# Kernel optimization log

Hardware: AMD Instinct MI355X
Metric: run time of the kernel (lower is better)

The kernel has to match this reference:

```python
import jax, jax.numpy as jnp
import numpy as np

B, T, C = 2, 2048, 2048
N_HEAD = 16
N_KV_HEAD = 16
HEAD_DIM = C // N_HEAD  # 128
KV_LORA = C // 2        # 1024
KV_PE = KV_LORA // 4    # 256
KV_CONTENT = KV_LORA - KV_PE  # 768
EPS = 1.1920929e-07  # torch.finfo(float32).eps, F.rms_norm default


def _rms_norm(x):
    # unlearned RMSNorm over last dim
    return x * jax.lax.rsqrt(jnp.mean(x * x, axis=-1, keepdims=True) + EPS)


def _apply_rotary(x, cos, sin):
    # x: (B,T,H,D); cos,sin: (1,T,1,D/2)
    d = x.shape[-1] // 2
    x1, x2 = x[..., :d], x[..., d:]
    return jnp.concatenate([x1 * cos + x2 * sin, -x1 * sin + x2 * cos], axis=-1)


def setup_inputs() -> dict:
    key = jax.random.key(0)
    ks = jax.random.split(key, 9)
    x = jax.random.normal(ks[0], (B, T, C), dtype=jnp.float32)
    # realistic RoPE tables (values bounded like real cos/sin)
    half = HEAD_DIM // 2
    inv_freq = 1.0 / (10000.0 ** (np.arange(0, half, dtype=np.float32) / half))
    tpos = np.arange(T, dtype=np.float32)
    ang = np.einsum('t,d->td', tpos, inv_freq)
    cos = jnp.asarray(np.cos(ang))[None, :, None, :]
    sin = jnp.asarray(np.sin(ang))[None, :, None, :]
    s = 0.02
    wq_a = jax.random.normal(ks[1], (C, KV_LORA), dtype=jnp.float32) * s
    wq_b = jax.random.normal(ks[2], (KV_LORA, N_HEAD * HEAD_DIM), dtype=jnp.float32) * s
    wkv_a = jax.random.normal(ks[3], (C, KV_LORA), dtype=jnp.float32) * s
    wk_b = jax.random.normal(ks[4], (KV_CONTENT, N_KV_HEAD * HEAD_DIM), dtype=jnp.float32) * s
    wkpe_b = jax.random.normal(ks[5], (KV_PE, N_KV_HEAD * HEAD_DIM), dtype=jnp.float32) * s
    wv_b = jax.random.normal(ks[6], (KV_CONTENT, N_KV_HEAD * HEAD_DIM), dtype=jnp.float32) * s
    wo = jax.random.normal(ks[7], (C, C), dtype=jnp.float32) * s
    return dict(x=x, cos=cos, sin=sin, wq_a=wq_a, wq_b=wq_b, wkv_a=wkv_a,
                wk_b=wk_b, wkpe_b=wkpe_b, wv_b=wv_b, wo=wo)


def reference(x, cos, sin, wq_a, wq_b, wkv_a, wk_b, wkpe_b, wv_b, wo):
    Bx, Tx, Cx = x.shape
    # low-rank Q path
    q = (x @ wq_a) @ wq_b                      # (B,T,H*D)
    q = q.reshape(Bx, Tx, N_HEAD, HEAD_DIM)
    # low-rank KV path with pe/content split
    kv_latent = x @ wkv_a                       # (B,T,KV_LORA)
    kv_pe = kv_latent[..., :KV_PE]
    kv_content = kv_latent[..., KV_PE:]
    k_content = (kv_content @ wk_b).reshape(Bx, Tx, N_KV_HEAD, HEAD_DIM)
    k_pe = (kv_pe @ wkpe_b).reshape(Bx, Tx, N_KV_HEAD, HEAD_DIM)
    k = k_content + _apply_rotary(k_pe, cos, sin)
    v = (kv_content @ wv_b).reshape(Bx, Tx, N_KV_HEAD, HEAD_DIM)
    # QK RMSNorm (unlearned)
    q = _rms_norm(q)
    k = _rms_norm(k)
    # SDPA, causal (kv_cache=None path); n_head == n_kv_head
    qh = q.transpose(0, 2, 1, 3)  # (B,H,T,D)
    kh = k.transpose(0, 2, 1, 3)
    vh = v.transpose(0, 2, 1, 3)
    scale = 1.0 / jnp.sqrt(jnp.asarray(HEAD_DIM, dtype=x.dtype))
    scores = jnp.einsum('bhqd,bhkd->bhqk', qh, kh) * scale
    causal = jnp.tril(jnp.ones((Tx, Tx), dtype=bool))
    scores = jnp.where(causal[None, None], scores, jnp.asarray(-jnp.inf, dtype=scores.dtype))
    probs = jax.nn.softmax(scores, axis=-1)
    y = jnp.einsum('bhqk,bhkd->bhqd', probs, vh)
    y = y.transpose(0, 2, 1, 3).reshape(Bx, Tx, Cx)
    return y @ wo
```

## Files before the change

### kernel.cpp

```cpp
#include <hip/hip_runtime.h>
#include <cstddef>
#include <cstdint>

#define TT 2048
#define HH 16
#define EPSV 1.1920929e-07f
#define QSCALE 0.08838834764831845f
#define LOG2E 1.4426950408889634f
#define THRL 11.0f

typedef short bfv8 __attribute__((ext_vector_type(8)));
typedef float f32x4 __attribute__((ext_vector_type(4)));

__device__ __forceinline__ short f2bf(float f) {
    unsigned u = __builtin_bit_cast(unsigned, f);
    u += 0x7FFFu + ((u >> 16) & 1u);
    return (short)(u >> 16);
}
__device__ __forceinline__ float bf2f(short s) {
    unsigned u = ((unsigned)(unsigned short)s) << 16;
    return __builtin_bit_cast(float, u);
}
__device__ __forceinline__ bfv8 pack8(const float4 a, const float4 b) {
    bfv8 r;
    r[0]=f2bf(a.x); r[1]=f2bf(a.y); r[2]=f2bf(a.z); r[3]=f2bf(a.w);
    r[4]=f2bf(b.x); r[5]=f2bf(b.y); r[6]=f2bf(b.z); r[7]=f2bf(b.w);
    return r;
}
__device__ __forceinline__ void gload16(const void* g, void* l) {
    __builtin_amdgcn_global_load_lds(
        (const __attribute__((address_space(1))) unsigned int*)g,
        (__attribute__((address_space(3))) unsigned int*)l, 16, 0, 0);
}
__device__ __forceinline__ unsigned cvtpk(float a, float b) {
    unsigned r;
    asm("v_cvt_pk_bf16_f32 %0, %1, %2" : "=v"(r) : "v"(a), "v"(b));
    return r;
}
__device__ __forceinline__ float fexp2(float x) {
    float y;
    asm volatile("v_exp_f32 %0, %1\n\ts_nop 1" : "=v"(y) : "v"(x));
    return y;
}
#define SWZF(V, IMM) __builtin_bit_cast(float, __builtin_amdgcn_ds_swizzle(__builtin_bit_cast(int, (V)), IMM))
#define RMAX_RND(M, IMM) { M[0]=fmaxf(M[0],SWZF(M[0],IMM)); M[1]=fmaxf(M[1],SWZF(M[1],IMM)); \
                           M[2]=fmaxf(M[2],SWZF(M[2],IMM)); M[3]=fmaxf(M[3],SWZF(M[3],IMM)); }
#define RMAX4(M) RMAX_RND(M,0x041F) RMAX_RND(M,0x081F) RMAX_RND(M,0x101F) RMAX_RND(M,0x201F)
#define RSUM_RND(M, IMM) { M[0]+=SWZF(M[0],IMM); M[1]+=SWZF(M[1],IMM); \
                           M[2]+=SWZF(M[2],IMM); M[3]+=SWZF(M[3],IMM); }
#define RSUM4(M) RSUM_RND(M,0x041F) RSUM_RND(M,0x081F) RSUM_RND(M,0x101F) RSUM_RND(M,0x201F)

__global__ __launch_bounds__(256) void convx(const float* __restrict__ src,
                                             short* __restrict__ dst, int n8)
{
    int i = blockIdx.x * blockDim.x + threadIdx.x;
    int stride = gridDim.x * blockDim.x;
    for (; i < n8; i += stride) {
        float4 a = ((const float4*)src)[2*i], b = ((const float4*)src)[2*i+1];
        ((bfv8*)dst)[i] = pack8(a, b);
    }
}

__global__ __launch_bounds__(256) void wtrans(const float* __restrict__ src,
                                              short* __restrict__ dst, int R, int C)
{
    __shared__ short tile[64][72];
    const int tid = threadIdx.x;
    const int r0 = blockIdx.y * 64, c0 = blockIdx.x * 64;
    {
        const int i = tid >> 2, c = (tid & 3) * 16;
        const float* sp = src + ((size_t)(r0 + i)) * C + c0 + c;
        float4 v0 = ((const float4*)sp)[0], v1 = ((const float4*)sp)[1];
        float4 v2 = ((const float4*)sp)[2], v3 = ((const float4*)sp)[3];
        *(bfv8*)&tile[i][c]     = pack8(v0, v1);
        *(bfv8*)&tile[i][c + 8] = pack8(v2, v3);
    }
    __syncthreads();
    {
        const int j = tid >> 2, rc = (tid & 3) * 16;
        bfv8 g0, g1;
#pragma unroll
        for (int jj = 0; jj < 8; ++jj) { g0[jj] = tile[rc + jj][j]; g1[jj] = tile[rc + 8 + jj][j]; }
        short* dp = dst + ((size_t)(c0 + j)) * R + r0 + rc;
        *(bfv8*)dp       = g0;
        *(bfv8*)(dp + 8) = g1;
    }
}

template<int OUT_MODE>
__global__ __launch_bounds__(256) void gemm_bf16(
    const short* __restrict__ A, int lda,
    const short* __restrict__ B, int ldb,
    void* __restrict__ Cptr, int ldc, int K)
{
    __shared__ short As[2][128 * 32];
    __shared__ short Bs[2][128 * 32];
    const int tid = threadIdx.x;
    const int w = tid >> 6, lane = tid & 63;
    const int lr = lane & 15, lg = lane >> 4;
    const int wr = w >> 1, wc = w & 1;
    const size_t bm = (size_t)blockIdx.y * 128, bn = (size_t)blockIdx.x * 128;

    f32x4 acc[4][4] = {};

    const int r0 = tid >> 2, ch = (tid & 3) * 8;
    const short* aB0 = A + (bm + r0) * (size_t)lda + ch;
    const short* aB1 = aB0 + 64 * (size_t)lda;
    const short* bB0 = B + (bn + r0) * (size_t)ldb + ch;
    const short* bB1 = bB0 + 64 * (size_t)ldb;
    const int wof = w * 512;

    gload16(aB0, As[0] + wof);
    gload16(aB1, As[0] + wof + 2048);
    gload16(bB0, Bs[0] + wof);
    gload16(bB1, Bs[0] + wof + 2048);
    __syncthreads();

    int cur = 0;
    for (int k0 = 0; k0 < K; k0 += 32) {
        if (k0 + 32 < K) {
            gload16(aB0 + k0 + 32, As[cur ^ 1] + wof);
            gload16(aB1 + k0 + 32, As[cur ^ 1] + wof + 2048);
            gload16(bB0 + k0 + 32, Bs[cur ^ 1] + wof);
            gload16(bB1 + k0 + 32, Bs[cur ^ 1] + wof + 2048);
        }
        bfv8 af[4], bfr[4];
#pragma unroll
        for (int i = 0; i < 4; ++i) {
            af[i]  = *(const bfv8*)&As[cur][(wr * 64 + i * 16 + lr) * 32 + lg * 8];
            bfr[i] = *(const bfv8*)&Bs[cur][(wc * 64 + i * 16 + lr) * 32 + lg * 8];
        }
#pragma unroll
        for (int i = 0; i < 4; ++i)
#pragma unroll
            for (int j = 0; j < 4; ++j)
                acc[i][j] = __builtin_amdgcn_mfma_f32_16x16x32_bf16(af[i], bfr[j], acc[i][j], 0, 0, 0);
        __syncthreads();
        cur ^= 1;
    }

    const size_t crow = bm + wr * 64 + 4 * lg;
    const size_t ccol = bn + wc * 64 + lr;
#pragma unroll
    for (int i = 0; i < 4; ++i)
#pragma unroll
        for (int j = 0; j < 4; ++j)
#pragma unroll
            for (int r = 0; r < 4; ++r) {
                size_t off = (crow + i * 16 + r) * (size_t)ldc + ccol + j * 16;
                if (OUT_MODE == 0) ((float*)Cptr)[off] = acc[i][j][r];
                else               ((short*)Cptr)[off] = f2bf(acc[i][j][r]);
            }
}

__global__ __launch_bounds__(256) void finalize_k(
    const short* __restrict__ kc, const short* __restrict__ pe,
    const float* __restrict__ cosb, const float* __restrict__ sinb,
    short* __restrict__ kb)
{
    const int gw = blockIdx.x * 4 + (threadIdx.x >> 6);
    const int l = threadIdx.x & 63;
    const int r = gw >> 4, h = gw & 15;
    const int t = r & (TT - 1), b = r >> 11;
    const size_t kcb = (size_t)r * 4096 + h * 128;
    const size_t peb = (size_t)r * 2048 + h * 128;

    float x1 = bf2f(pe[peb + l]), x2 = bf2f(pe[peb + 64 + l]);
    float c = cosb[t * 64 + l], s = sinb[t * 64 + l];
    float lo = bf2f(kc[kcb + l])      + x1 * c + x2 * s;
    float hi = bf2f(kc[kcb + 64 + l]) - x1 * s + x2 * c;

    float ss = lo * lo + hi * hi;
#pragma unroll
    for (int o = 32; o; o >>= 1) ss += __shfl_xor(ss, o);
    float rr = rsqrtf(ss * (1.0f / 128.0f) + EPSV);
    const size_t ob = (((size_t)b * HH + h) * TT + t) * 128;
    kb[ob + l]      = f2bf(lo * rr);
    kb[ob + 64 + l] = f2bf(hi * rr);
}

__global__ __launch_bounds__(256) void vtrans(
    const short* __restrict__ src, short* __restrict__ dst)
{
    __shared__ short tile[64][72];
    const int tt = blockIdx.x, dt = blockIdx.y, bh = blockIdx.z;
    const int tid = threadIdx.x;
    {
        const int i = tid >> 2, c = (tid & 3) * 16;
        const size_t sb = ((size_t)((bh >> 4) * TT + tt * 64 + i)) * 4096 + 2048 + (bh & 15) * 128 + dt * 64 + c;
        *(bfv8*)&tile[i][c]     = *(const bfv8*)&src[sb];
        *(bfv8*)&tile[i][c + 8] = *(const bfv8*)&src[sb + 8];
    }
    __syncthreads();
    {
        const int j = tid >> 2, rc = (tid & 3) * 16;
        bfv8 g0, g1;
#pragma unroll
        for (int jj = 0; jj < 8; ++jj) { g0[jj] = tile[rc + jj][j]; g1[jj] = tile[rc + 8 + jj][j]; }
        const size_t db = (((size_t)bh) * 128 + dt * 64 + j) * TT + tt * 64 + rc;
        *(bfv8*)&dst[db]     = g0;
        *(bfv8*)&dst[db + 8] = g1;
    }
}

__device__ __forceinline__ void qk_tile(const short* __restrict__ Ks,
    const bfv8 aq[4], f32x4 s[4], int lr, int lg)
{
    const int swz = lr & 7;
#pragma unroll
    for (int ct = 0; ct < 4; ++ct) {
        f32x4 a = {0.f, 0.f, 0.f, 0.f};
        const int row = ct * 16 + lr;
#pragma unroll
        for (int ks = 0; ks < 4; ++ks) {
            const bfv8 bk = *(const bfv8*)&Ks[row * 128 + (((ks * 4 + lg) ^ swz) * 8)];
            a = __builtin_amdgcn_mfma_f32_16x16x32_bf16(aq[ks], bk, a, 0, 0, 0);
        }
        s[ct] = a;
    }
}

__device__ __forceinline__ void mask_diag(f32x4 s[4], int lr, int lg, int w)
{
    const int rq = w * 16 + 4 * lg;
#pragma unroll
    for (int ct = 0; ct < 4; ++ct)
#pragma unroll
        for (int r = 0; r < 4; ++r)
            if (ct * 16 + lr > rq + r) s[ct][r] = -__builtin_inff();
}

__device__ __forceinline__ void softmax1(f32x4 s[4], float m[4], float l[4], f32x4 o[8])
{
    float mt[4];
#pragma unroll
    for (int r = 0; r < 4; ++r) mt[r] = fmaxf(fmaxf(s[0][r], s[1][r]), fmaxf(s[2][r], s[3][r]));
    RMAX4(mt)
    float g = fmaxf(fmaxf(mt[0] - m[0], mt[1] - m[1]), fmaxf(mt[2] - m[2], mt[3] - m[3]));
    if (!__all(g <= THRL)) {
        float alpha[4];
#pragma unroll
        for (int r = 0; r < 4; ++r) {
            float mn = fmaxf(m[r], mt[r]);
            alpha[r] = fexp2(m[r] - mn);
            m[r] = mn; l[r] *= alpha[r];
        }
#pragma unroll
        for (int dt = 0; dt < 8; ++dt) {
            o[dt][0] *= alpha[0]; o[dt][1] *= alpha[1];
            o[dt][2] *= alpha[2]; o[dt][3] *= alpha[3];
        }
    }
#pragma unroll
    for (int ct = 0; ct < 4; ++ct)
#pragma unroll
        for (int r = 0; r < 4; ++r) s[ct][r] = fexp2(s[ct][r] - m[r]);
    float rs[4];
#pragma unroll
    for (int r = 0; r < 4; ++r) rs[r] = (s[0][r] + s[1][r]) + (s[2][r] + s[3][r]);
    RSUM4(rs)
#pragma unroll
    for (int r = 0; r < 4; ++r) l[r] += rs[r];
}

__device__ __forceinline__ void softmax2(
    f32x4 s1[4], f32x4 s2[4],
    float m1[4], float l1[4], float m2[4], float l2[4],
    f32x4 o1[8], f32x4 o2[8])
{
    float mt1[4], mt2[4];
#pragma unroll
    for (int r = 0; r < 4; ++r) {
        mt1[r] = fmaxf(fmaxf(s1[0][r], s1[1][r]), fmaxf(s1[2][r], s1[3][r]));
        mt2[r] = fmaxf(fmaxf(s2[0][r], s2[1][r]), fmaxf(s2[2][r], s2[3][r]));
    }
    RMAX4(mt1) RMAX4(mt2)
    float g1 = fmaxf(fmaxf(mt1[0] - m1[0], mt1[1] - m1[1]), fmaxf(mt1[2] - m1[2], mt1[3] - m1[3]));
    float g2 = fmaxf(fmaxf(mt2[0] - m2[0], mt2[1] - m2[1]), fmaxf(mt2[2] - m2[2], mt2[3] - m2[3]));
    if (!__all(g1 <= THRL)) {
        float alpha[4];
#pragma unroll
        for (int r = 0; r < 4; ++r) {
            float mn = fmaxf(m1[r], mt1[r]);
            alpha[r] = fexp2(m1[r] - mn);
            m1[r] = mn; l1[r] *= alpha[r];
        }
#pragma unroll
        for (int dt = 0; dt < 8; ++dt) {
            o1[dt][0] *= alpha[0]; o1[dt][1] *= alpha[1];
            o1[dt][2] *= alpha[2]; o1[dt][3] *= alpha[3];
        }
    }
    if (!__all(g2 <= THRL)) {
        float alpha[4];
#pragma unroll
        for (int r = 0; r < 4; ++r) {
            float mn = fmaxf(m2[r], mt2[r]);
            alpha[r] = fexp2(m2[r] - mn);
            m2[r] = mn; l2[r] *= alpha[r];
        }
#pragma unroll
        for (int dt = 0; dt < 8; ++dt) {
            o2[dt][0] *= alpha[0]; o2[dt][1] *= alpha[1];
            o2[dt][2] *= alpha[2]; o2[dt][3] *= alpha[3];
        }
    }
#pragma unroll
    for (int ct = 0; ct < 4; ++ct)
#pragma unroll
        for (int r = 0; r < 4; ++r) {
            s1[ct][r] = fexp2(s1[ct][r] - m1[r]);
            s2[ct][r] = fexp2(s2[ct][r] - m2[r]);
        }
    float rs1[4], rs2[4];
#pragma unroll
    for (int r = 0; r < 4; ++r) {
        rs1[r] = (s1[0][r] + s1[1][r]) + (s1[2][r] + s1[3][r]);
        rs2[r] = (s2[0][r] + s2[1][r]) + (s2[2][r] + s2[3][r]);
    }
    RSUM4(rs1) RSUM4(rs2)
#pragma unroll
    for (int r = 0; r < 4; ++r) { l1[r] += rs1[r]; l2[r] += rs2[r]; }
}

__device__ __forceinline__ void pv_tile(const short* __restrict__ Vs,
    short (&Psw)[16][72], const f32x4 s[4], f32x4 o[8], int lr, int lg)
{
#pragma unroll
    for (int ct = 0; ct < 4; ++ct) {
        unsigned u0 = cvtpk(s[ct][0], s[ct][1]);
        unsigned u1 = cvtpk(s[ct][2], s[ct][3]);
        Psw[4 * lg + 0][ct * 16 + lr] = (short)u0;
        Psw[4 * lg + 1][ct * 16 + lr] = (short)(u0 >> 16);
        Psw[4 * lg + 2][ct * 16 + lr] = (short)u1;
        Psw[4 * lg + 3][ct * 16 + lr] = (short)(u1 >> 16);
    }
    const bfv8 pa0 = *(const bfv8*)&Psw[lr][lg * 8];
    const bfv8 pa1 = *(const bfv8*)&Psw[lr][32 + lg * 8];
    const int swz = lr & 7;
#pragma unroll
    for (int dt = 0; dt < 8; ++dt) {
        const int row = dt * 16 + lr;
        const bfv8 bv0 = *(const bfv8*)&Vs[row * 64 + ((lg ^ swz) * 8)];
        const bfv8 bv1 = *(const bfv8*)&Vs[row * 64 + (((4 + lg) ^ swz) * 8)];
        o[dt] = __builtin_amdgcn_mfma_f32_16x16x32_bf16(pa0, bv0, o[dt], 0, 0, 0);
        o[dt] = __builtin_amdgcn_mfma_f32_16x16x32_bf16(pa1, bv1, o[dt], 0, 0, 0);
    }
}

__global__ __launch_bounds__(256) void attn_kernel(
    const short* __restrict__ qg, const short* __restrict__ kg,
    const short* __restrict__ vg, short* __restrict__ y)
{
    __shared__ short Ks[64 * 128];
    __shared__ short Vs[128 * 64];
    __shared__ short Ps[4][16][72];

    const int lin = blockIdx.x + 16 * blockIdx.y + 256 * blockIdx.z;
    const int work = (lin & 7) * 64 + (lin >> 3);
    const int pi = work & 15, h = (work >> 4) & 15, b = work >> 8;
    const int qt1 = pi, qt2 = 31 - pi;
    const int tid = threadIdx.x, w = tid >> 6, lane = tid & 63;
    const int lr = lane & 15, lg = lane >> 4;

    const size_t tok0 = ((size_t)b * HH + h) * TT;

    bfv8 aq1[4], aq2[4];
    {
        const size_t q1 = ((size_t)b * TT + qt1 * 64 + w * 16 + lr) * 2048 + h * 128;
        const size_t q2 = ((size_t)b * TT + qt2 * 64 + w * 16 + lr) * 2048 + h * 128;
#pragma unroll
        for (int ks = 0; ks < 4; ++ks) {
            aq1[ks] = *(const bfv8*)&qg[q1 + ks * 32 + lg * 8];
            aq2[ks] = *(const bfv8*)&qg[q2 + ks * 32 + lg * 8];
        }
#pragma unroll
        for (int st = 0; st < 2; ++st) {
            bfv8* aq = st ? aq2 : aq1;
            float ss = 0.f;
#pragma unroll
            for (int ks = 0; ks < 4; ++ks)
#pragma unroll
                for (int j = 0; j < 8; ++j) { float f = bf2f(aq[ks][j]); ss = fmaf(f, f, ss); }
            ss += __shfl_xor(ss, 16);
            ss += __shfl_xor(ss, 32);
            float rr = rsqrtf(ss * (1.0f / 128.0f) + EPSV) * (QSCALE * LOG2E);
#pragma unroll
            for (int ks = 0; ks < 4; ++ks)
#pragma unroll
                for (int j = 0; j < 4; ++j) {
                    unsigned u = cvtpk(bf2f(aq[ks][2 * j]) * rr, bf2f(aq[ks][2 * j + 1]) * rr);
                    aq[ks][2 * j]     = (short)u;
                    aq[ks][2 * j + 1] = (short)(u >> 16);
                }
        }
    }

    f32x4 o1[8] = {}; f32x4 o2[8] = {};
    float m1[4], l1[4], m2[4], l2[4];
#pragma unroll
    for (int r = 0; r < 4; ++r) { m1[r] = m2[r] = -__builtin_inff(); l1[r] = l2[r] = 0.f; }

    const size_t vhead = ((size_t)b * HH + h) * (size_t)128 * TT;
    const int krow = tid >> 4, kub = (tid & 15) ^ (krow & 7);
    const int vrow = tid >> 3, vub = (tid & 7) ^ (vrow & 7);
    const int wof = w * 512;

    for (int kt = 0; kt <= qt2; ++kt) {
        {
            const size_t kbase = (tok0 + kt * 64) * 128;
#pragma unroll
            for (int p = 0; p < 4; ++p) {
                gload16(kg + kbase + (p * 16 + krow) * 128 + kub * 8, Ks + wof + p * 2048);
                gload16(vg + vhead + (size_t)(p * 32 + vrow) * TT + kt * 64 + vub * 8,
                        Vs + wof + p * 2048);
            }
        }
        __syncthreads();

        if (kt <= qt1) {
            f32x4 s1[4], s2[4];
            qk_tile(Ks, aq2, s2, lr, lg);
            qk_tile(Ks, aq1, s1, lr, lg);
            if (kt == qt1) mask_diag(s1, lr, lg, w);
            softmax2(s1, s2, m1, l1, m2, l2, o1, o2);
            pv_tile(Vs, Ps[w], s2, o2, lr, lg);
            pv_tile(Vs, Ps[w], s1, o1, lr, lg);
        } else {
            f32x4 s2[4];
            qk_tile(Ks, aq2, s2, lr, lg);
            if (kt == qt2) mask_diag(s2, lr, lg, w);
            softmax1(s2, m2, l2, o2);
            pv_tile(Vs, Ps[w], s2, o2, lr, lg);
        }
        __syncthreads();
    }

#pragma unroll
    for (int r = 0; r < 4; ++r) {
        float inv1 = 1.0f / l1[r], inv2 = 1.0f / l2[r];
        const size_t y1 = ((size_t)b * TT + qt1 * 64 + w * 16 + 4 * lg + r) * 2048 + h * 128 + lr;
        const size_t y2 = ((size_t)b * TT + qt2 * 64 + w * 16 + 4 * lg + r) * 2048 + h * 128 + lr;
#pragma unroll
        for (int dt = 0; dt < 8; ++dt) {
            y[y1 + dt * 16] = f2bf(o1[dt][r] * inv1);
            y[y2 + dt * 16] = f2bf(o2[dt][r] * inv2);
        }
    }
}

extern "C" void kernel_launch(void* const* d_in, const int* in_sizes, int n_in,
                              void* d_out, int out_size, void* d_ws, size_t ws_size,
                              hipStream_t stream)
{
    const float* x      = (const float*)d_in[0];
    const float* cosb   = (const float*)d_in[1];
    const float* sinb   = (const float*)d_in[2];
    const float* wq_a   = (const float*)d_in[3];
    const float* wq_b   = (const float*)d_in[4];
    const float* wkv_a  = (const float*)d_in[5];
    const float* wk_b   = (const float*)d_in[6];
    const float* wkpe_b = (const float*)d_in[7];
    const float* wv_b   = (const float*)d_in[8];
    const float* wo     = (const float*)d_in[9];

    short* wsp = (short*)d_ws;
    short* W1  = wsp;
    short* W2  = wsp + 4194304;
    short* W3  = wsp + 7340032;
    short* W4  = wsp + 7864320;
    short* W5  = wsp + 9961472;
    short* C1  = wsp + 14155776;
    short* KV2 = wsp + 22544384;
    short* KPE = wsp + 39321600;
    short* KB  = wsp + 47710208;
    short* VB  = wsp + 56098816;
    short* XB  = (short*)d_out;

    dim3 blk(256);

    convx<<<2048, blk, 0, stream>>>(x, XB, 1048576);
    wtrans<<<dim3(16, 32), blk, 0, stream>>>(wq_a,   W1,                2048, 1024);
    wtrans<<<dim3(16, 32), blk, 0, stream>>>(wkv_a,  W1 + 1024 * 2048,  2048, 1024);
    wtrans<<<dim3(32, 12), blk, 0, stream>>>(wk_b,   W2,                 768, 2048);
    wtrans<<<dim3(32, 12), blk, 0, stream>>>(wv_b,   W2 + 2048 * 768,    768, 2048);
    wtrans<<<dim3(32,  4), blk, 0, stream>>>(wkpe_b, W3,                 256, 2048);
    wtrans<<<dim3(32, 16), blk, 0, stream>>>(wq_b,   W4,                1024, 2048);
    wtrans<<<dim3(32, 32), blk, 0, stream>>>(wo,     W5,                2048, 2048);

    gemm_bf16<1><<<dim3(16, 32), blk, 0, stream>>>(XB, 2048, W1, 2048, C1, 2048, 2048);
    gemm_bf16<1><<<dim3(32, 32), blk, 0, stream>>>(C1 + 1280, 2048, W2, 768, KV2, 4096, 768);
    gemm_bf16<1><<<dim3(16, 32), blk, 0, stream>>>(C1 + 1024, 2048, W3, 256, KPE, 2048, 256);

    finalize_k<<<16384, blk, 0, stream>>>(KV2, KPE, cosb, sinb, KB);
    vtrans<<<dim3(32, 2, 32), blk, 0, stream>>>(KV2, VB);

    gemm_bf16<1><<<dim3(16, 32), blk, 0, stream>>>(C1, 2048, W4, 1024, KPE, 2048, 1024);

    attn_kernel<<<dim3(16, 16, 2), blk, 0, stream>>>(KPE, KB, VB, C1);

    gemm_bf16<0><<<dim3(16, 32), blk, 0, stream>>>(C1, 2048, W5, 2048, d_out, 2048, 2048);
}
```

Before: 348.9 us.

## Transpose QK MFMA so each lane owns one query row in softmax

The QK^T MFMA operands are swapped so the score tile comes out transposed, with each lane holding one query row across four key columns. Row max and sum then need only two cross-lane shuffles instead of four swizzle rounds per row, and P is stored to LDS as packed 4-element vectors. The rescale factors and final normalisers are redistributed to the O-accumulator layout with ds_bpermute. Separate P buffers per query tile let both PV products run interleaved in one loop, which adds LDS use and extra permutes on rescale.

```diff
diff --git a/kernel.cpp b/kernel.cpp
--- a/kernel.cpp
+++ b/kernel.cpp
@@ -10,7 +10,9 @@
 #define THRL 11.0f
 
 typedef short bfv8 __attribute__((ext_vector_type(8)));
+typedef short bfv4 __attribute__((ext_vector_type(4)));
 typedef float f32x4 __attribute__((ext_vector_type(4)));
+typedef unsigned u32x2 __attribute__((ext_vector_type(2)));
 
 __device__ __forceinline__ short f2bf(float f) {
     unsigned u = __builtin_bit_cast(unsigned, f);
@@ -42,13 +44,14 @@
     asm volatile("v_exp_f32 %0, %1\n\ts_nop 1" : "=v"(y) : "v"(x));
     return y;
 }
-#define SWZF(V, IMM) __builtin_bit_cast(float, __builtin_amdgcn_ds_swizzle(__builtin_bit_cast(int, (V)), IMM))
-#define RMAX_RND(M, IMM) { M[0]=fmaxf(M[0],SWZF(M[0],IMM)); M[1]=fmaxf(M[1],SWZF(M[1],IMM)); \
-                           M[2]=fmaxf(M[2],SWZF(M[2],IMM)); M[3]=fmaxf(M[3],SWZF(M[3],IMM)); }
-#define RMAX4(M) RMAX_RND(M,0x041F) RMAX_RND(M,0x081F) RMAX_RND(M,0x101F) RMAX_RND(M,0x201F)
-#define RSUM_RND(M, IMM) { M[0]+=SWZF(M[0],IMM); M[1]+=SWZF(M[1],IMM); \
-                           M[2]+=SWZF(M[2],IMM); M[3]+=SWZF(M[3],IMM); }
-#define RSUM4(M) RSUM_RND(M,0x041F) RSUM_RND(M,0x081F) RSUM_RND(M,0x101F) RSUM_RND(M,0x201F)
+__device__ __forceinline__ float bperm(float v, int addr) {
+    return __builtin_bit_cast(float,
+        __builtin_amdgcn_ds_bpermute(addr, __builtin_bit_cast(int, v)));
+}
+__device__ __forceinline__ bfv4 mkfrag(float a, float b, float c, float d) {
+    u32x2 t; t[0] = cvtpk(a, b); t[1] = cvtpk(c, d);
+    return __builtin_bit_cast(bfv4, t);
+}
 
 __global__ __launch_bounds__(256) void convx(const float* __restrict__ src,
                                              short* __restrict__ dst, int n8)
@@ -203,7 +206,25 @@
     }
 }
 
-__device__ __forceinline__ void qk_tile(const short* __restrict__ Ks,
+__device__ __forceinline__ void qk_dual(const short* __restrict__ Ks,
+    const bfv8 aq1[4], const bfv8 aq2[4], f32x4 s1[4], f32x4 s2[4], int lr, int lg)
+{
+    const int swz = lr & 7;
+#pragma unroll
+    for (int ct = 0; ct < 4; ++ct) {
+        f32x4 a1 = {0.f, 0.f, 0.f, 0.f}, a2 = {0.f, 0.f, 0.f, 0.f};
+        const int row = ct * 16 + lr;
+#pragma unroll
+        for (int ks = 0; ks < 4; ++ks) {
+            const bfv8 bk = *(const bfv8*)&Ks[row * 128 + (((ks * 4 + lg) ^ swz) * 8)];
+            a1 = __builtin_amdgcn_mfma_f32_16x16x32_bf16(bk, aq1[ks], a1, 0, 0, 0);
+            a2 = __builtin_amdgcn_mfma_f32_16x16x32_bf16(bk, aq2[ks], a2, 0, 0, 0);
+        }
+        s1[ct] = a1; s2[ct] = a2;
+    }
+}
+
+__device__ __forceinline__ void qk_one(const short* __restrict__ Ks,
     const bfv8 aq[4], f32x4 s[4], int lr, int lg)
 {
     const int swz = lr & 7;
@@ -214,7 +235,7 @@
 #pragma unroll
         for (int ks = 0; ks < 4; ++ks) {
             const bfv8 bk = *(const bfv8*)&Ks[row * 128 + (((ks * 4 + lg) ^ swz) * 8)];
-            a = __builtin_amdgcn_mfma_f32_16x16x32_bf16(aq[ks], bk, a, 0, 0, 0);
+            a = __builtin_amdgcn_mfma_f32_16x16x32_bf16(bk, aq[ks], a, 0, 0, 0);
         }
         s[ct] = a;
     }
@@ -222,121 +243,86 @@
 
 __device__ __forceinline__ void mask_diag(f32x4 s[4], int lr, int lg, int w)
 {
-    const int rq = w * 16 + 4 * lg;
+    const int qq = w * 16 + lr;
 #pragma unroll
     for (int ct = 0; ct < 4; ++ct)
 #pragma unroll
         for (int r = 0; r < 4; ++r)
-            if (ct * 16 + lr > rq + r) s[ct][r] = -__builtin_inff();
-}
-
-__device__ __forceinline__ void softmax1(f32x4 s[4], float m[4], float l[4], f32x4 o[8])
-{
-    float mt[4];
-#pragma unroll
-    for (int r = 0; r < 4; ++r) mt[r] = fmaxf(fmaxf(s[0][r], s[1][r]), fmaxf(s[2][r], s[3][r]));
-    RMAX4(mt)
-    float g = fmaxf(fmaxf(mt[0] - m[0], mt[1] - m[1]), fmaxf(mt[2] - m[2], mt[3] - m[3]));
-    if (!__all(g <= THRL)) {
-        float alpha[4];
-#pragma unroll
-        for (int r = 0; r < 4; ++r) {
-            float mn = fmaxf(m[r], mt[r]);
-            alpha[r] = fexp2(m[r] - mn);
-            m[r] = mn; l[r] *= alpha[r];
-        }
+            if (ct * 16 + 4 * lg + r > qq) s[ct][r] = -__builtin_inff();
+}
+
+__device__ __forceinline__ void softmax_lane(f32x4 s[4], float& m, float& l,
+                                             f32x4 o[8], int a0)
+{
+    float c0 = fmaxf(fmaxf(s[0][0], s[0][1]), fmaxf(s[0][2], s[0][3]));
+    float c1 = fmaxf(fmaxf(s[1][0], s[1][1]), fmaxf(s[1][2], s[1][3]));
+    float c2 = fmaxf(fmaxf(s[2][0], s[2][1]), fmaxf(s[2][2], s[2][3]));
+    float c3 = fmaxf(fmaxf(s[3][0], s[3][1]), fmaxf(s[3][2], s[3][3]));
+    float mt = fmaxf(fmaxf(c0, c1), fmaxf(c2, c3));
+    mt = fmaxf(mt, __shfl_xor(mt, 16));
+    mt = fmaxf(mt, __shfl_xor(mt, 32));
+    if (!__all(mt - m <= THRL)) {
+        float mn = fmaxf(m, mt);
+        float alpha = fexp2(m - mn);
+        m = mn;
+        l *= alpha;
+        float av0 = bperm(alpha, a0);
+        float av1 = bperm(alpha, a0 + 4);
+        float av2 = bperm(alpha, a0 + 8);
+        float av3 = bperm(alpha, a0 + 12);
 #pragma unroll
         for (int dt = 0; dt < 8; ++dt) {
-            o[dt][0] *= alpha[0]; o[dt][1] *= alpha[1];
-            o[dt][2] *= alpha[2]; o[dt][3] *= alpha[3];
-        }
-    }
+            o[dt][0] *= av0; o[dt][1] *= av1;
+            o[dt][2] *= av2; o[dt][3] *= av3;
+        }
+    }
+    f32x4 acc = {0.f, 0.f, 0.f, 0.f};
+#pragma unroll
+    for (int ct = 0; ct < 4; ++ct) {
+#pragma unroll
+        for (int r = 0; r < 4; ++r) s[ct][r] = fexp2(s[ct][r] - m);
+        acc += s[ct];
+    }
+    float rs = (acc[0] + acc[1]) + (acc[2] + acc[3]);
+    rs += __shfl_xor(rs, 16);
+    rs += __shfl_xor(rs, 32);
+    l += rs;
+}
+
+__device__ __forceinline__ void p_store(short (&Psw)[16][72], const f32x4 s[4],
+                                        int lr, int lg)
+{
 #pragma unroll
     for (int ct = 0; ct < 4; ++ct)
-#pragma unroll
-        for (int r = 0; r < 4; ++r) s[ct][r] = fexp2(s[ct][r] - m[r]);
-    float rs[4];
-#pragma unroll
-    for (int r = 0; r < 4; ++r) rs[r] = (s[0][r] + s[1][r]) + (s[2][r] + s[3][r]);
-    RSUM4(rs)
-#pragma unroll
-    for (int r = 0; r < 4; ++r) l[r] += rs[r];
-}
-
-__device__ __forceinline__ void softmax2(
-    f32x4 s1[4], f32x4 s2[4],
-    float m1[4], float l1[4], float m2[4], float l2[4],
-    f32x4 o1[8], f32x4 o2[8])
-{
-    float mt1[4], mt2[4];
-#pragma unroll
-    for (int r = 0; r < 4; ++r) {
-        mt1[r] = fmaxf(fmaxf(s1[0][r], s1[1][r]), fmaxf(s1[2][r], s1[3][r]));
-        mt2[r] = fmaxf(fmaxf(s2[0][r], s2[1][r]), fmaxf(s2[2][r], s2[3][r]));
-    }
-    RMAX4(mt1) RMAX4(mt2)
-    float g1 = fmaxf(fmaxf(mt1[0] - m1[0], mt1[1] - m1[1]), fmaxf(mt1[2] - m1[2], mt1[3] - m1[3]));
-    float g2 = fmaxf(fmaxf(mt2[0] - m2[0], mt2[1] - m2[1]), fmaxf(mt2[2] - m2[2], mt2[3] - m2[3]));
-    if (!__all(g1 <= THRL)) {
-        float alpha[4];
-#pragma unroll
-        for (int r = 0; r < 4; ++r) {
-            float mn = fmaxf(m1[r], mt1[r]);
-            alpha[r] = fexp2(m1[r] - mn);
-            m1[r] = mn; l1[r] *= alpha[r];
-        }
-#pragma unroll
-        for (int dt = 0; dt < 8; ++dt) {
-            o1[dt][0] *= alpha[0]; o1[dt][1] *= alpha[1];
-            o1[dt][2] *= alpha[2]; o1[dt][3] *= alpha[3];
-        }
-    }
-    if (!__all(g2 <= THRL)) {
-        float alpha[4];
-#pragma unroll
-        for (int r = 0; r < 4; ++r) {
-            float mn = fmaxf(m2[r], mt2[r]);
-            alpha[r] = fexp2(m2[r] - mn);
-            m2[r] = mn; l2[r] *= alpha[r];
-        }
-#pragma unroll
-        for (int dt = 0; dt < 8; ++dt) {
-            o2[dt][0] *= alpha[0]; o2[dt][1] *= alpha[1];
-            o2[dt][2] *= alpha[2]; o2[dt][3] *= alpha[3];
-        }
-    }
-#pragma unroll
-    for (int ct = 0; ct < 4; ++ct)
-#pragma unroll
-        for (int r = 0; r < 4; ++r) {
-            s1[ct][r] = fexp2(s1[ct][r] - m1[r]);
-            s2[ct][r] = fexp2(s2[ct][r] - m2[r]);
-        }
-    float rs1[4], rs2[4];
-#pragma unroll
-    for (int r = 0; r < 4; ++r) {
-        rs1[r] = (s1[0][r] + s1[1][r]) + (s1[2][r] + s1[3][r]);
-        rs2[r] = (s2[0][r] + s2[1][r]) + (s2[2][r] + s2[3][r]);
-    }
-    RSUM4(rs1) RSUM4(rs2)
-#pragma unroll
-    for (int r = 0; r < 4; ++r) { l1[r] += rs1[r]; l2[r] += rs2[r]; }
-}
-
-__device__ __forceinline__ void pv_tile(const short* __restrict__ Vs,
-    short (&Psw)[16][72], const f32x4 s[4], f32x4 o[8], int lr, int lg)
-{
-#pragma unroll
-    for (int ct = 0; ct < 4; ++ct) {
-        unsigned u0 = cvtpk(s[ct][0], s[ct][1]);
-        unsigned u1 = cvtpk(s[ct][2], s[ct][3]);
-        Psw[4 * lg + 0][ct * 16 + lr] = (short)u0;
-        Psw[4 * lg + 1][ct * 16 + lr] = (short)(u0 >> 16);
-        Psw[4 * lg + 2][ct * 16 + lr] = (short)u1;
-        Psw[4 * lg + 3][ct * 16 + lr] = (short)(u1 >> 16);
-    }
-    const bfv8 pa0 = *(const bfv8*)&Psw[lr][lg * 8];
-    const bfv8 pa1 = *(const bfv8*)&Psw[lr][32 + lg * 8];
+        *(bfv4*)&Psw[lr][ct * 16 + 4 * lg] = mkfrag(s[ct][0], s[ct][1], s[ct][2], s[ct][3]);
+}
+
+__device__ __forceinline__ void pv_dual(const short* __restrict__ Vs,
+    const short (&P1)[16][72], const short (&P2)[16][72],
+    f32x4 o1[8], f32x4 o2[8], int lr, int lg)
+{
+    const bfv8 pa0 = *(const bfv8*)&P1[lr][lg * 8];
+    const bfv8 pa1 = *(const bfv8*)&P1[lr][32 + lg * 8];
+    const bfv8 pb0 = *(const bfv8*)&P2[lr][lg * 8];
+    const bfv8 pb1 = *(const bfv8*)&P2[lr][32 + lg * 8];
+    const int swz = lr & 7;
+#pragma unroll
+    for (int dt = 0; dt < 8; ++dt) {
+        const int row = dt * 16 + lr;
+        const bfv8 bv0 = *(const bfv8*)&Vs[row * 64 + ((lg ^ swz) * 8)];
+        const bfv8 bv1 = *(const bfv8*)&Vs[row * 64 + (((4 + lg) ^ swz) * 8)];
+        o1[dt] = __builtin_amdgcn_mfma_f32_16x16x32_bf16(pa0, bv0, o1[dt], 0, 0, 0);
+        o1[dt] = __builtin_amdgcn_mfma_f32_16x16x32_bf16(pa1, bv1, o1[dt], 0, 0, 0);
+        o2[dt] = __builtin_amdgcn_mfma_f32_16x16x32_bf16(pb0, bv0, o2[dt], 0, 0, 0);
+        o2[dt] = __builtin_amdgcn_mfma_f32_16x16x32_bf16(pb1, bv1, o2[dt], 0, 0, 0);
+    }
+}
+
+__device__ __forceinline__ void pv_one(const short* __restrict__ Vs,
+    const short (&P2)[16][72], f32x4 o[8], int lr, int lg)
+{
+    const bfv8 pa0 = *(const bfv8*)&P2[lr][lg * 8];
+    const bfv8 pa1 = *(const bfv8*)&P2[lr][32 + lg * 8];
     const int swz = lr & 7;
 #pragma unroll
     for (int dt = 0; dt < 8; ++dt) {
@@ -354,7 +340,8 @@
 {
     __shared__ short Ks[64 * 128];
     __shared__ short Vs[128 * 64];
-    __shared__ short Ps[4][16][72];
+    __shared__ short Ps1[4][16][72];
+    __shared__ short Ps2[4][16][72];
 
     const int lin = blockIdx.x + 16 * blockIdx.y + 256 * blockIdx.z;
     const int work = (lin & 7) * 64 + (lin >> 3);
@@ -362,6 +349,7 @@
     const int qt1 = pi, qt2 = 31 - pi;
     const int tid = threadIdx.x, w = tid >> 6, lane = tid & 63;
     const int lr = lane & 15, lg = lane >> 4;
+    const int a0 = lg * 80;
 
     const size_t tok0 = ((size_t)b * HH + h) * TT;
 
@@ -397,9 +385,8 @@
     }
 
     f32x4 o1[8] = {}; f32x4 o2[8] = {};
-    float m1[4], l1[4], m2[4], l2[4];
-#pragma unroll
-    for (int r = 0; r < 4; ++r) { m1[r] = m2[r] = -__builtin_inff(); l1[r] = l2[r] = 0.f; }
+    float m1 = -__builtin_inff(), m2 = -__builtin_inff();
+    float l1 = 0.f, l2 = 0.f;
 
     const size_t vhead = ((size_t)b * HH + h) * (size_t)128 * TT;
     const int krow = tid >> 4, kub = (tid & 15) ^ (krow & 7);
@@ -420,31 +407,39 @@
 
         if (kt <= qt1) {
             f32x4 s1[4], s2[4];
-            qk_tile(Ks, aq2, s2, lr, lg);
-            qk_tile(Ks, aq1, s1, lr, lg);
+            qk_dual(Ks, aq1, aq2, s1, s2, lr, lg);
             if (kt == qt1) mask_diag(s1, lr, lg, w);
-            softmax2(s1, s2, m1, l1, m2, l2, o1, o2);
-            pv_tile(Vs, Ps[w], s2, o2, lr, lg);
-            pv_tile(Vs, Ps[w], s1, o1, lr, lg);
+            softmax_lane(s1, m1, l1, o1, a0);
+            softmax_lane(s2, m2, l2, o2, a0);
+            p_store(Ps1[w], s1, lr, lg);
+            p_store(Ps2[w], s2, lr, lg);
+            pv_dual(Vs, Ps1[w], Ps2[w], o1, o2, lr, lg);
         } else {
             f32x4 s2[4];
-            qk_tile(Ks, aq2, s2, lr, lg);
+            qk_one(Ks, aq2, s2, lr, lg);
             if (kt == qt2) mask_diag(s2, lr, lg, w);
-            softmax1(s2, m2, l2, o2);
-            pv_tile(Vs, Ps[w], s2, o2, lr, lg);
+            softmax_lane(s2, m2, l2, o2, a0);
+            p_store(Ps2[w], s2, lr, lg);
+            pv_one(Vs, Ps2[w], o2, lr, lg);
         }
         __syncthreads();
     }
 
+    float n1 = 1.0f / l1, n2 = 1.0f / l2;
+    float iv1[4], iv2[4];
 #pragma unroll
     for (int r = 0; r < 4; ++r) {
-        float inv1 = 1.0f / l1[r], inv2 = 1.0f / l2[r];
+        iv1[r] = bperm(n1, a0 + 4 * r);
+        iv2[r] = bperm(n2, a0 + 4 * r);
+    }
+#pragma unroll
+    for (int r = 0; r < 4; ++r) {
         const size_t y1 = ((size_t)b * TT + qt1 * 64 + w * 16 + 4 * lg + r) * 2048 + h * 128 + lr;
         const size_t y2 = ((size_t)b * TT + qt2 * 64 + w * 16 + 4 * lg + r) * 2048 + h * 128 + lr;
 #pragma unroll
         for (int dt = 0; dt < 8; ++dt) {
-            y[y1 + dt * 16] = f2bf(o1[dt][r] * inv1);
-            y[y2 + dt * 16] = f2bf(o2[dt][r] * inv2);
+            y[y1 + dt * 16] = f2bf(o1[dt][r] * iv1[r]);
+            y[y2 + dt * 16] = f2bf(o2[dt][r] * iv2[r]);
         }
     }
 }
```

New measurement: 334.9 us. 1.04x faster.
